# Optimization experiments

Measured on AMD Instinct MI355X. Metric: run time of the kernel, lower is better.

The kernel has to match this reference:

```python
import jax, jax.numpy as jnp
import numpy as np

WINDOW = 7
TOKEN_SELF_ATTN_VALUE = -5e4  # from lucidrains local-attention
LN_EPS = 1e-5


def _layer_norm(x, g, b):
    mu = jnp.mean(x, axis=-1, keepdims=True)
    var = jnp.mean(jnp.square(x - mu), axis=-1, keepdims=True)
    return (x - mu) * jax.lax.rsqrt(var + LN_EPS) * g + b


def _local_attention(q, k, v, window):
    # q,k,v: (b, n, d); shared_qk=True, causal=True, look_backward=1, look_forward=0
    b, n, d = q.shape
    nw = n // window
    scale = d ** -0.5
    # shared_qk: l2-normalize keys (torch F.normalize eps=1e-12)
    k = k / jnp.maximum(jnp.linalg.norm(k, axis=-1, keepdims=True), 1e-12)
    bq = q.reshape(b, nw, window, d) * scale
    bk = k.reshape(b, nw, window, d)
    bv = v.reshape(b, nw, window, d)
    # look_around: previous window + current window -> (b, nw, 2w, d)
    prev_k = jnp.pad(bk, ((0, 0), (1, 0), (0, 0), (0, 0)))[:, :nw]
    prev_v = jnp.pad(bv, ((0, 0), (1, 0), (0, 0), (0, 0)))[:, :nw]
    bk2 = jnp.concatenate([prev_k, bk], axis=2)
    bv2 = jnp.concatenate([prev_v, bv], axis=2)
    # absolute positions; padded positions marked -1
    t = jnp.arange(n).reshape(nw, window)             # (nw, w)
    prev_t = jnp.pad(t, ((1, 0), (0, 0)), constant_values=-1)[:nw]
    tk = jnp.concatenate([prev_t, t], axis=1)          # (nw, 2w)
    sim = jnp.einsum('bnie,bnje->bnij', bq, bk2)       # (b, nw, w, 2w)
    self_mask = t[:, :, None] == tk[:, None, :]
    sim = jnp.where(self_mask, TOKEN_SELF_ATTN_VALUE, sim)
    invalid = (t[:, :, None] < tk[:, None, :]) | (tk[:, None, :] == -1)
    sim = jnp.where(invalid, -jnp.finfo(sim.dtype).max, sim)
    attn = jax.nn.softmax(sim, axis=-1)
    out = jnp.einsum('bnij,bnjd->bnid', attn, bv2)
    return out.reshape(b, n, d)


def setup_inputs() -> dict:
    key = jax.random.key(0)
    ks = jax.random.split(key, 10)
    B, H, W, C = 8, 112, 112, 256
    s = 1.0 / np.sqrt(C)
    return {
        'x': jax.random.normal(ks[0], (B, H, W, C), dtype=jnp.float32),
        'ln_g': jnp.ones((C,), jnp.float32),
        'ln_b': jnp.zeros((C,), jnp.float32),
        'wq_w': jax.random.uniform(ks[1], (C, C), jnp.float32, -s, s),
        'wq_b': jax.random.uniform(ks[2], (C,), jnp.float32, -s, s),
        'wk_w': jax.random.uniform(ks[3], (C, C), jnp.float32, -s, s),
        'wk_b': jax.random.uniform(ks[4], (C,), jnp.float32, -s, s),
        'wv_w': jax.random.uniform(ks[5], (C, C), jnp.float32, -s, s),
        'wv_b': jax.random.uniform(ks[6], (C,), jnp.float32, -s, s),
        'mlp_w': jax.random.uniform(ks[7], (C, C), jnp.float32, -s, s),
        'mlp_b': jax.random.uniform(ks[8], (C,), jnp.float32, -s, s),
    }


def reference(x, ln_g, ln_b, wq_w, wq_b, wk_w, wk_b, wv_w, wv_b, mlp_w, mlp_b):
    B, H, W, C = x.shape
    shift = WINDOW // 2  # int(7/2) = 3
    xs = jnp.roll(x, (shift, shift), axis=(1, 2))
    xs = _layer_norm(xs, ln_g, ln_b)
    flat = xs.reshape(B, H * W, C)
    q = flat @ wq_w.T + wq_b
    k = flat @ wk_w.T + wk_b
    v = flat @ wv_w.T + wv_b
    attn_out = _local_attention(q, k, v, WINDOW).reshape(B, H, W, C)
    x_unshifted = jnp.roll(attn_out, (-shift, -shift), axis=(1, 2))
    residual = x_unshifted + x
    xn = _layer_norm(residual, ln_g, ln_b)  # same LN params (module reused)
    flat2 = xn.reshape(B, H * W, C)
    mlp = jax.nn.gelu(flat2 @ mlp_w.T + mlp_b, approximate=False).reshape(B, H, W, C)
    return mlp + residual
```

## Files before the change

kernel.cpp:

```cpp
#include <hip/hip_runtime.h>

#define NTOK 100352
#define NPB  12544
#define CH   256

typedef unsigned short u16;
typedef float f32x4 __attribute__((ext_vector_type(4)));
typedef short bfrag __attribute__((ext_vector_type(8)));

static __device__ __forceinline__ u16 f2bf(float f) {
    union { float f; unsigned u; } v; v.f = f;
    unsigned r = v.u + 0x7FFFu + ((v.u >> 16) & 1u);
    return (u16)(r >> 16);
}
static __device__ __forceinline__ float bf2f(u16 h) {
    union { unsigned u; float f; } v; v.u = ((unsigned)h) << 16;
    return v.f;
}
static __device__ __forceinline__ unsigned pk2(float a, float b) {
    return (unsigned)f2bf(a) | ((unsigned)f2bf(b) << 16);
}

__global__ __launch_bounds__(256)
void swa_prep(const float* __restrict__ wq, const float* __restrict__ wk,
              const float* __restrict__ wv, const float* __restrict__ wm,
              u16* __restrict__ wcat, u16* __restrict__ wmb)
{
    int i0 = blockIdx.x * 256 + threadIdx.x;
    int stride = gridDim.x * 256;
    for (int i = i0; i < 768 * 256; i += stride) {
        int r = i >> 8, c = i & 255;
        float v;
        if (r < 256)      v = wq[r * 256 + c] * 0.0625f;
        else if (r < 512) v = wk[(r - 256) * 256 + c];
        else              v = wv[(r - 512) * 256 + c];
        wcat[i] = f2bf(v);
    }
    for (int i = i0; i < 256 * 256; i += stride) wmb[i] = f2bf(wm[i]);
}

__global__ __launch_bounds__(256)
void swa_ln(const float* __restrict__ x,
            const float* __restrict__ ln_g, const float* __restrict__ ln_b,
            u16* __restrict__ xn)
{
    const int lane = threadIdx.x & 63;
    const int wid  = threadIdx.x >> 6;
    f32x4 lg = *reinterpret_cast<const f32x4*>(ln_g + lane * 4);
    f32x4 lb = *reinterpret_cast<const f32x4*>(ln_b + lane * 4);

    const int wtok0 = (blockIdx.x * 4 + wid) * 16;
    for (int i = 0; i < 16; ++i) {
        int tok = wtok0 + i;
        int b_  = tok / NPB;
        int rem = tok - b_ * NPB;
        int h = rem / 112, w = rem - h * 112;
        int h0 = h - 3 + ((h < 3) ? 112 : 0);
        int w0 = w - 3 + ((w < 3) ? 112 : 0);
        f32x4 v = *reinterpret_cast<const f32x4*>(x + (size_t)(b_ * NPB + h0 * 112 + w0) * CH + lane * 4);
        float s  = v[0] + v[1] + v[2] + v[3];
        float sq = v[0]*v[0] + v[1]*v[1] + v[2]*v[2] + v[3]*v[3];
        #pragma unroll
        for (int m = 1; m < 64; m <<= 1) { s += __shfl_xor(s, m); sq += __shfl_xor(sq, m); }
        float mu  = s * (1.0f / 256.0f);
        float var = sq * (1.0f / 256.0f) - mu * mu;
        float inv = 1.0f / sqrtf(var + 1e-5f);
        uint2 p;
        p.x = pk2((v[0] - mu) * inv * lg[0] + lb[0], (v[1] - mu) * inv * lg[1] + lb[1]);
        p.y = pk2((v[2] - mu) * inv * lg[2] + lb[2], (v[3] - mu) * inv * lg[3] + lb[3]);
        *reinterpret_cast<uint2*>(xn + (size_t)tok * CH + lane * 4) = p;
    }
}

__global__ __launch_bounds__(256)
void swa_qkv6(const u16* __restrict__ xn, const u16* __restrict__ wcat,
              const float* __restrict__ bq, const float* __restrict__ bk,
              const float* __restrict__ bv,
              u16* __restrict__ qbuf, u16* __restrict__ kbuf, u16* __restrict__ vbuf)
{
    __shared__ u16 wt[2][64 * 64];

    const int tid  = threadIdx.x;
    const int lane = tid & 63;
    const int wid  = tid >> 6;
    const int r16  = lane & 15, g4 = lane >> 4;
    const int swz  = (blockIdx.x & 7) * 98 + (blockIdx.x >> 3);
    const int tok0 = swz * 128;
    const int trow0 = wid * 32;

    bfrag bx[2][8];
    #pragma unroll
    for (int fj = 0; fj < 2; ++fj) {
        const u16* xp = xn + (size_t)(tok0 + trow0 + fj * 16 + r16) * CH + g4 * 8;
        #pragma unroll
        for (int kk = 0; kk < 8; ++kk)
            bx[fj][kk] = *reinterpret_cast<const bfrag*>(xp + kk * 32);
    }

    uint4 wreg[2];
    auto wload = [&](int s) {
        int pp = s >> 2, t = s & 3;
        #pragma unroll
        for (int it = 0; it < 2; ++it) {
            int cid = tid + it * 256;
            int row = cid >> 3, c = cid & 7;
            wreg[it] = *reinterpret_cast<const uint4*>(wcat + (size_t)(pp * 64 + row) * CH + t * 64 + c * 8);
        }
    };
    auto wstore = [&](int p) {
        char* d = (char*)wt[p];
        #pragma unroll
        for (int it = 0; it < 2; ++it) {
            int cid = tid + it * 256;
            int row = cid >> 3, c = cid & 7;
            *reinterpret_cast<uint4*>(d + row * 128 + ((c ^ (row & 7)) << 4)) = wreg[it];
        }
    };

    wload(0); wstore(0);
    __syncthreads();

    f32x4 acc[4][2];
    #pragma unroll
    for (int fi = 0; fi < 4; ++fi) { acc[fi][0] = (f32x4)0.f; acc[fi][1] = (f32x4)0.f; }

    for (int pp = 0; pp < 12; ++pp) {
        #pragma unroll
        for (int t = 0; t < 4; ++t) {
            const int s = pp * 4 + t;
            const int p = s & 1;
            if (s < 47) wload(s + 1);
            const char* wp = (const char*)wt[p];
            #pragma unroll
            for (int kk = 0; kk < 2; ++kk) {
                bfrag af[4];
                #pragma unroll
                for (int fi = 0; fi < 4; ++fi) {
                    int row = fi * 16 + r16;
                    af[fi] = *reinterpret_cast<const bfrag*>(wp + row * 128 + (((kk * 4 + g4) ^ (row & 7)) << 4));
                }
                #pragma unroll
                for (int fi = 0; fi < 4; ++fi)
                    #pragma unroll
                    for (int fj = 0; fj < 2; ++fj)
                        acc[fi][fj] = __builtin_amdgcn_mfma_f32_16x16x32_bf16(af[fi], bx[fj][t * 2 + kk], acc[fi][fj], 0, 0, 0);
            }
            if (t == 3) {
                const int sec = pp >> 2;
                u16* outp = (sec == 0) ? qbuf : (sec == 1) ? kbuf : vbuf;
                const float* bp = (sec == 0) ? bq : (sec == 1) ? bk : bv;
                const float bscale = (sec == 0) ? 0.0625f : 1.0f;
                #pragma unroll
                for (int fi = 0; fi < 4; ++fi) {
                    int chl = (pp & 3) * 64 + fi * 16 + g4 * 4;
                    f32x4 bb = *reinterpret_cast<const f32x4*>(bp + chl);
                    #pragma unroll
                    for (int fj = 0; fj < 2; ++fj) {
                        int tok = tok0 + trow0 + fj * 16 + r16;
                        uint2 pk;
                        pk.x = pk2(acc[fi][fj][0] + bb[0] * bscale, acc[fi][fj][1] + bb[1] * bscale);
                        pk.y = pk2(acc[fi][fj][2] + bb[2] * bscale, acc[fi][fj][3] + bb[3] * bscale);
                        *reinterpret_cast<uint2*>(outp + (size_t)tok * CH + chl) = pk;
                        acc[fi][fj] = (f32x4)0.f;
                    }
                }
            }
            if (s < 47) wstore(p ^ 1);
            __syncthreads();
        }
    }
}

__global__ __launch_bounds__(256)
void swa_attn(const u16* qbuf, const u16* kbuf, const u16* vbuf, u16* obuf)
{
    __shared__ float plds[4][16][17];
    const int tid  = threadIdx.x;
    const int lane = tid & 63;
    const int wid  = tid >> 6;
    const int win  = blockIdx.x * 4 + wid;
    const int iw   = win % 1792;
    const int base = win * 7;
    const int r16  = lane & 15;
    const int g4   = lane >> 4;

    int qrow = base + r16; if (qrow > NTOK - 1) qrow = NTOK - 1;
    int krow = base - 7 + r16; if (krow < 0) krow = 0;
    const u16* qp = qbuf + (size_t)qrow * CH + g4 * 8;
    const u16* kp = kbuf + (size_t)krow * CH + g4 * 8;

    bfrag kf[8];
    #pragma unroll
    for (int kk = 0; kk < 8; ++kk) kf[kk] = *reinterpret_cast<const bfrag*>(kp + kk * 32);
    float sq = 0.f;
    #pragma unroll
    for (int kk = 0; kk < 8; ++kk)
        #pragma unroll
        for (int e = 0; e < 8; ++e) { float kv = bf2f((u16)kf[kk][e]); sq += kv * kv; }
    sq += __shfl_xor(sq, 16); sq += __shfl_xor(sq, 32);
    float invk = 1.0f / fmaxf(sqrtf(sq), 1e-12f);

    f32x4 s4 = {0.f, 0.f, 0.f, 0.f};
    #pragma unroll
    for (int kk = 0; kk < 8; ++kk) {
        bfrag a = *reinterpret_cast<const bfrag*>(qp + kk * 32);
        s4 = __builtin_amdgcn_mfma_f32_16x16x32_bf16(a, kf[kk], s4, 0, 0, 0);
    }

    const int  j     = r16;
    const bool first = (iw == 0);
    #pragma unroll
    for (int rr = 0; rr < 4; ++rr) {
        int i = g4 * 4 + rr;
        float s = s4[rr] * invk;
        if (j == i + 7) s = -5.0e4f;
        if (j > i + 7 || j >= 14 || (first && j < 7)) s = -3.0e38f;
        s4[rr] = s;
    }
    f32x4 mx = s4;
    #pragma unroll
    for (int off = 8; off; off >>= 1) {
        #pragma unroll
        for (int rr = 0; rr < 4; ++rr) mx[rr] = fmaxf(mx[rr], __shfl_xor(mx[rr], off));
    }
    f32x4 p;
    #pragma unroll
    for (int rr = 0; rr < 4; ++rr) p[rr] = __expf(s4[rr] - mx[rr]);
    f32x4 sm = p;
    #pragma unroll
    for (int off = 8; off; off >>= 1) {
        #pragma unroll
        for (int rr = 0; rr < 4; ++rr) sm[rr] += __shfl_xor(sm[rr], off);
    }
    #pragma unroll
    for (int rr = 0; rr < 4; ++rr) plds[wid][g4 * 4 + rr][j] = p[rr] / sm[rr];
    __syncthreads();

    f32x4 zero4 = {0.f, 0.f, 0.f, 0.f};
    f32x4 oa[7];
    #pragma unroll
    for (int i = 0; i < 7; ++i) oa[i] = zero4;
    for (int jj = 0; jj < 14; ++jj) {
        int vrow = base - 7 + jj;
        if (vrow < 0) vrow = 0;
        ushort4 vr = *reinterpret_cast<const ushort4*>(vbuf + (size_t)vrow * CH + lane * 4);
        f32x4 vvv; vvv[0] = bf2f(vr.x); vvv[1] = bf2f(vr.y); vvv[2] = bf2f(vr.z); vvv[3] = bf2f(vr.w);
        #pragma unroll
        for (int i = 0; i < 7; ++i) {
            float pp = plds[wid][i][jj];
            oa[i][0] += pp * vvv[0]; oa[i][1] += pp * vvv[1];
            oa[i][2] += pp * vvv[2]; oa[i][3] += pp * vvv[3];
        }
    }
    #pragma unroll
    for (int i = 0; i < 7; ++i) {
        ushort4 o; o.x = f2bf(oa[i][0]); o.y = f2bf(oa[i][1]); o.z = f2bf(oa[i][2]); o.w = f2bf(oa[i][3]);
        *reinterpret_cast<ushort4*>(obuf + (size_t)(base + i) * CH + lane * 4) = o;
    }
}

__global__ __launch_bounds__(256)
void swa_mlp4(const float* __restrict__ x, const u16* __restrict__ abuf,
              const float* __restrict__ ln_g, const float* __restrict__ ln_b,
              const u16* __restrict__ wmb, const float* __restrict__ mbias,
              float* __restrict__ out)
{
    __shared__ u16   xs[32][264];
    __shared__ float rsd[32][260];
    __shared__ float bias[256];
    const int tid  = threadIdx.x;
    const int lane = tid & 63;
    const int wid  = tid >> 6;
    const int tok0 = blockIdx.x * 32;
    const int r16  = lane & 15;
    const int g4   = lane >> 4;

    if (tid < 256) bias[tid] = mbias[tid];
    f32x4 lg = *reinterpret_cast<const f32x4*>(ln_g + lane * 4);
    f32x4 lb = *reinterpret_cast<const f32x4*>(ln_b + lane * 4);

    for (int it = 0; it < 8; ++it) {
        int tt  = wid * 8 + it;
        int tok = tok0 + tt;
        int b_  = tok / NPB, rem = tok - b_ * NPB;
        int h = rem / 112, w = rem - h * 112;
        int hs = h + 3;  if (hs >= 112) hs -= 112;
        int ws_ = w + 3; if (ws_ >= 112) ws_ -= 112;
        const u16* arow = abuf + (size_t)(b_ * NPB + hs * 112 + ws_) * CH;
        ushort4 av = *reinterpret_cast<const ushort4*>(arow + lane * 4);
        f32x4 xv = *reinterpret_cast<const f32x4*>(x + (size_t)tok * CH + lane * 4);
        f32x4 rv;
        rv[0] = xv[0] + bf2f(av.x); rv[1] = xv[1] + bf2f(av.y);
        rv[2] = xv[2] + bf2f(av.z); rv[3] = xv[3] + bf2f(av.w);
        *reinterpret_cast<f32x4*>(&rsd[tt][lane * 4]) = rv;
        float s  = rv[0] + rv[1] + rv[2] + rv[3];
        float sq = rv[0]*rv[0] + rv[1]*rv[1] + rv[2]*rv[2] + rv[3]*rv[3];
        #pragma unroll
        for (int m = 32; m; m >>= 1) { s += __shfl_xor(s, m); sq += __shfl_xor(sq, m); }
        float mu  = s * (1.0f / 256.0f);
        float var = sq * (1.0f / 256.0f) - mu * mu;
        float inv = 1.0f / sqrtf(var + 1e-5f);
        ushort4 o;
        o.x = f2bf((rv[0] - mu) * inv * lg[0] + lb[0]);
        o.y = f2bf((rv[1] - mu) * inv * lg[1] + lb[1]);
        o.z = f2bf((rv[2] - mu) * inv * lg[2] + lb[2]);
        o.w = f2bf((rv[3] - mu) * inv * lg[3] + lb[3]);
        *reinterpret_cast<ushort4*>(&xs[tt][lane * 4]) = o;
    }
    __syncthreads();

    f32x4 acc[4][2];
    #pragma unroll
    for (int i = 0; i < 4; ++i) { acc[i][0] = (f32x4)0.f; acc[i][1] = (f32x4)0.f; }

    #pragma unroll
    for (int kk = 0; kk < 8; ++kk) {
        bfrag b0 = *reinterpret_cast<const bfrag*>(&xs[r16][kk * 32 + g4 * 8]);
        bfrag b1 = *reinterpret_cast<const bfrag*>(&xs[16 + r16][kk * 32 + g4 * 8]);
        #pragma unroll
        for (int ct = 0; ct < 4; ++ct) {
            bfrag wf = *reinterpret_cast<const bfrag*>(wmb + (size_t)(wid * 64 + ct * 16 + r16) * CH + kk * 32 + g4 * 8);
            acc[ct][0] = __builtin_amdgcn_mfma_f32_16x16x32_bf16(wf, b0, acc[ct][0], 0, 0, 0);
            acc[ct][1] = __builtin_amdgcn_mfma_f32_16x16x32_bf16(wf, b1, acc[ct][1], 0, 0, 0);
        }
    }

    #pragma unroll
    for (int ct = 0; ct < 4; ++ct) {
        int ch = wid * 64 + ct * 16 + g4 * 4;
        f32x4 bb = *reinterpret_cast<const f32x4*>(&bias[ch]);
        #pragma unroll
        for (int rt = 0; rt < 2; ++rt) {
            int tokL = rt * 16 + r16;
            f32x4 rb = *reinterpret_cast<const f32x4*>(&rsd[tokL][ch]);
            f32x4 vv;
            #pragma unroll
            for (int rr = 0; rr < 4; ++rr) {
                float val = acc[ct][rt][rr] + bb[rr];
                vv[rr] = 0.5f * val * (1.0f + erff(val * 0.70710678118654752f)) + rb[rr];
            }
            *reinterpret_cast<f32x4*>(out + (size_t)(tok0 + tokL) * CH + ch) = vv;
        }
    }
}

extern "C" void kernel_launch(void* const* d_in, const int* in_sizes, int n_in,
                              void* d_out, int out_size, void* d_ws, size_t ws_size,
                              hipStream_t stream)
{
    const float* x     = (const float*)d_in[0];
    const float* ln_g  = (const float*)d_in[1];
    const float* ln_b  = (const float*)d_in[2];
    const float* wq_w  = (const float*)d_in[3];
    const float* wq_b  = (const float*)d_in[4];
    const float* wk_w  = (const float*)d_in[5];
    const float* wk_b  = (const float*)d_in[6];
    const float* wv_w  = (const float*)d_in[7];
    const float* wv_b  = (const float*)d_in[8];
    const float* mlp_w = (const float*)d_in[9];
    const float* mlp_b = (const float*)d_in[10];

    char* ws = (char*)d_ws;
    u16* wcat = (u16*)ws;
    u16* wmb  = (u16*)(ws + 393216);
    u16* xnq  = (u16*)(ws + 524288);
    u16* kbuf = (u16*)d_out;
    u16* vbuf = (u16*)d_out + (size_t)NTOK * CH;

    swa_prep <<<256,  256, 0, stream>>>(wq_w, wk_w, wv_w, mlp_w, wcat, wmb);
    swa_ln   <<<1568, 256, 0, stream>>>(x, ln_g, ln_b, xnq);
    swa_qkv6 <<<784,  256, 0, stream>>>(xnq, wcat, wq_b, wk_b, wv_b, xnq, kbuf, vbuf);
    swa_attn <<<3584, 256, 0, stream>>>(xnq, kbuf, vbuf, xnq);
    swa_mlp4 <<<3136, 256, 0, stream>>>(x, xnq, ln_g, ln_b, wmb, mlp_b, (float*)d_out);
}
```

Baseline: 305.2 us.

## Restructure QKV GEMM with direct global-to-LDS weight staging and 512-thread blocks

```diff
diff --git a/kernel.cpp b/kernel.cpp
--- a/kernel.cpp
+++ b/kernel.cpp
@@ -19,6 +19,11 @@
 }
 static __device__ __forceinline__ unsigned pk2(float a, float b) {
     return (unsigned)f2bf(a) | ((unsigned)f2bf(b) << 16);
+}
+static __device__ __forceinline__ void gl16(const u16* g, u16* l) {
+    __builtin_amdgcn_global_load_lds(
+        (const __attribute__((address_space(1))) void*)g,
+        (__attribute__((address_space(3))) void*)l, 16, 0, 0);
 }
 
 __global__ __launch_bounds__(256)
@@ -72,102 +77,106 @@
     }
 }
 
-__global__ __launch_bounds__(256)
-void swa_qkv6(const u16* __restrict__ xn, const u16* __restrict__ wcat,
+#define QSTEP(KH, SPP, DOSTAGE)                                                        \
+    {                                                                                  \
+        if (DOSTAGE) {                                                                 \
+            const int spp_ = (SPP);                                                    \
+            _Pragma("unroll")                                                          \
+            for (int it = 0; it < 2; ++it) {                                           \
+                int o   = (tid + it * 512) * 16;                                       \
+                int row = o >> 8;                                                      \
+                int cp  = (o >> 4) & 15;                                               \
+                int c   = (cp & 8) | ((cp & 7) ^ (row & 7));                           \
+                const u16* gp = wcat + (size_t)(spp_ * 64 + row) * CH + ((KH) ^ 1) * 128 + c * 8; \
+                gl16(gp, (u16*)wt[(KH) ^ 1] + o / 2);                                  \
+            }                                                                          \
+        }                                                                              \
+        const char* wp = (const char*)wt[(KH)];                                        \
+        _Pragma("unroll")                                                              \
+        for (int kk = 0; kk < 4; ++kk) {                                               \
+            bfrag af[2];                                                               \
+            _Pragma("unroll")                                                          \
+            for (int fi = 0; fi < 2; ++fi) {                                           \
+                int row = wch * 32 + fi * 16 + r16;                                    \
+                int cc  = kk * 4 + g4;                                                 \
+                int cp  = (cc & 8) | ((cc & 7) ^ (r16 & 7));                           \
+                af[fi]  = *reinterpret_cast<const bfrag*>(wp + row * 256 + cp * 16);   \
+            }                                                                          \
+            _Pragma("unroll")                                                          \
+            for (int fi = 0; fi < 2; ++fi)                                             \
+                _Pragma("unroll")                                                      \
+                for (int fj = 0; fj < 2; ++fj)                                         \
+                    acc[fi][fj] = __builtin_amdgcn_mfma_f32_16x16x32_bf16(af[fi], bx[fj][(KH) * 4 + kk], acc[fi][fj], 0, 0, 0); \
+        }                                                                              \
+    }
+
+__global__ __launch_bounds__(512)
+void swa_qkv7(const u16* __restrict__ xn, const u16* __restrict__ wcat,
               const float* __restrict__ bq, const float* __restrict__ bk,
               const float* __restrict__ bv,
               u16* __restrict__ qbuf, u16* __restrict__ kbuf, u16* __restrict__ vbuf)
 {
-    __shared__ u16 wt[2][64 * 64];
+    __shared__ u16 wt[2][64 * 128];
 
     const int tid  = threadIdx.x;
     const int lane = tid & 63;
     const int wid  = tid >> 6;
     const int r16  = lane & 15, g4 = lane >> 4;
+    const int wch  = wid & 1;
+    const int wtk  = wid >> 1;
     const int swz  = (blockIdx.x & 7) * 98 + (blockIdx.x >> 3);
     const int tok0 = swz * 128;
-    const int trow0 = wid * 32;
+    const int trow0 = wtk * 32;
 
     bfrag bx[2][8];
     #pragma unroll
     for (int fj = 0; fj < 2; ++fj) {
         const u16* xp = xn + (size_t)(tok0 + trow0 + fj * 16 + r16) * CH + g4 * 8;
         #pragma unroll
-        for (int kk = 0; kk < 8; ++kk)
-            bx[fj][kk] = *reinterpret_cast<const bfrag*>(xp + kk * 32);
-    }
-
-    uint4 wreg[2];
-    auto wload = [&](int s) {
-        int pp = s >> 2, t = s & 3;
-        #pragma unroll
-        for (int it = 0; it < 2; ++it) {
-            int cid = tid + it * 256;
-            int row = cid >> 3, c = cid & 7;
-            wreg[it] = *reinterpret_cast<const uint4*>(wcat + (size_t)(pp * 64 + row) * CH + t * 64 + c * 8);
-        }
-    };
-    auto wstore = [&](int p) {
-        char* d = (char*)wt[p];
-        #pragma unroll
-        for (int it = 0; it < 2; ++it) {
-            int cid = tid + it * 256;
-            int row = cid >> 3, c = cid & 7;
-            *reinterpret_cast<uint4*>(d + row * 128 + ((c ^ (row & 7)) << 4)) = wreg[it];
-        }
-    };
-
-    wload(0); wstore(0);
+        for (int kb = 0; kb < 8; ++kb)
+            bx[fj][kb] = *reinterpret_cast<const bfrag*>(xp + kb * 32);
+    }
+
+    #pragma unroll
+    for (int it = 0; it < 2; ++it) {
+        int o   = (tid + it * 512) * 16;
+        int row = o >> 8;
+        int cp  = (o >> 4) & 15;
+        int c   = (cp & 8) | ((cp & 7) ^ (row & 7));
+        gl16(wcat + (size_t)row * CH + c * 8, (u16*)wt[0] + o / 2);
+    }
     __syncthreads();
 
-    f32x4 acc[4][2];
-    #pragma unroll
-    for (int fi = 0; fi < 4; ++fi) { acc[fi][0] = (f32x4)0.f; acc[fi][1] = (f32x4)0.f; }
+    f32x4 acc[2][2];
+    #pragma unroll
+    for (int fi = 0; fi < 2; ++fi) { acc[fi][0] = (f32x4)0.f; acc[fi][1] = (f32x4)0.f; }
 
     for (int pp = 0; pp < 12; ++pp) {
-        #pragma unroll
-        for (int t = 0; t < 4; ++t) {
-            const int s = pp * 4 + t;
-            const int p = s & 1;
-            if (s < 47) wload(s + 1);
-            const char* wp = (const char*)wt[p];
+        QSTEP(0, pp, true);
+        __syncthreads();
+        QSTEP(1, pp + 1, pp < 11);
+
+        {
+            const int sec = pp >> 2;
+            u16* outp = (sec == 0) ? qbuf : (sec == 1) ? kbuf : vbuf;
+            const float* bp = (sec == 0) ? bq : (sec == 1) ? bk : bv;
+            const float bsc = (sec == 0) ? 0.0625f : 1.0f;
             #pragma unroll
-            for (int kk = 0; kk < 2; ++kk) {
-                bfrag af[4];
+            for (int fi = 0; fi < 2; ++fi) {
+                int chl = (pp & 3) * 64 + wch * 32 + fi * 16 + g4 * 4;
+                f32x4 bb = *reinterpret_cast<const f32x4*>(bp + chl);
                 #pragma unroll
-                for (int fi = 0; fi < 4; ++fi) {
-                    int row = fi * 16 + r16;
-                    af[fi] = *reinterpret_cast<const bfrag*>(wp + row * 128 + (((kk * 4 + g4) ^ (row & 7)) << 4));
-                }
-                #pragma unroll
-                for (int fi = 0; fi < 4; ++fi)
-                    #pragma unroll
-                    for (int fj = 0; fj < 2; ++fj)
-                        acc[fi][fj] = __builtin_amdgcn_mfma_f32_16x16x32_bf16(af[fi], bx[fj][t * 2 + kk], acc[fi][fj], 0, 0, 0);
-            }
-            if (t == 3) {
-                const int sec = pp >> 2;
-                u16* outp = (sec == 0) ? qbuf : (sec == 1) ? kbuf : vbuf;
-                const float* bp = (sec == 0) ? bq : (sec == 1) ? bk : bv;
-                const float bscale = (sec == 0) ? 0.0625f : 1.0f;
-                #pragma unroll
-                for (int fi = 0; fi < 4; ++fi) {
-                    int chl = (pp & 3) * 64 + fi * 16 + g4 * 4;
-                    f32x4 bb = *reinterpret_cast<const f32x4*>(bp + chl);
-                    #pragma unroll
-                    for (int fj = 0; fj < 2; ++fj) {
-                        int tok = tok0 + trow0 + fj * 16 + r16;
-                        uint2 pk;
-                        pk.x = pk2(acc[fi][fj][0] + bb[0] * bscale, acc[fi][fj][1] + bb[1] * bscale);
-                        pk.y = pk2(acc[fi][fj][2] + bb[2] * bscale, acc[fi][fj][3] + bb[3] * bscale);
-                        *reinterpret_cast<uint2*>(outp + (size_t)tok * CH + chl) = pk;
-                        acc[fi][fj] = (f32x4)0.f;
-                    }
+                for (int fj = 0; fj < 2; ++fj) {
+                    int tok = tok0 + trow0 + fj * 16 + r16;
+                    uint2 pk;
+                    pk.x = pk2(acc[fi][fj][0] + bb[0] * bsc, acc[fi][fj][1] + bb[1] * bsc);
+                    pk.y = pk2(acc[fi][fj][2] + bb[2] * bsc, acc[fi][fj][3] + bb[3] * bsc);
+                    *reinterpret_cast<uint2*>(outp + (size_t)tok * CH + chl) = pk;
+                    acc[fi][fj] = (f32x4)0.f;
                 }
             }
-            if (s < 47) wstore(p ^ 1);
-            __syncthreads();
         }
+        __syncthreads();
     }
 }
 
@@ -369,7 +378,7 @@
 
     swa_prep <<<256,  256, 0, stream>>>(wq_w, wk_w, wv_w, mlp_w, wcat, wmb);
     swa_ln   <<<1568, 256, 0, stream>>>(x, ln_g, ln_b, xnq);
-    swa_qkv6 <<<784,  256, 0, stream>>>(xnq, wcat, wq_b, wk_b, wv_b, xnq, kbuf, vbuf);
+    swa_qkv7 <<<784,  512, 0, stream>>>(xnq, wcat, wq_b, wk_b, wv_b, xnq, kbuf, vbuf);
     swa_attn <<<3584, 256, 0, stream>>>(xnq, kbuf, vbuf, xnq);
     swa_mlp4 <<<3136, 256, 0, stream>>>(x, xnq, ln_g, ln_b, wmb, mlp_b, (float*)d_out);
 }
```

Result: faster. 282.4 us (-7.5%).

## Fuse LayerNorm into QKV projection and hold full weight section in LDS

Applied to the files above, without the earlier changes.

```diff
diff --git a/kernel.cpp b/kernel.cpp
--- a/kernel.cpp
+++ b/kernel.cpp
@@ -19,6 +19,11 @@
 }
 static __device__ __forceinline__ unsigned pk2(float a, float b) {
     return (unsigned)f2bf(a) | ((unsigned)f2bf(b) << 16);
+}
+static __device__ __forceinline__ void gl16(const u16* g, u16* l) {
+    __builtin_amdgcn_global_load_lds(
+        (const __attribute__((address_space(1))) void*)g,
+        (__attribute__((address_space(3))) void*)l, 16, 0, 0);
 }
 
 __global__ __launch_bounds__(256)
@@ -39,134 +44,116 @@
     for (int i = i0; i < 256 * 256; i += stride) wmb[i] = f2bf(wm[i]);
 }
 
-__global__ __launch_bounds__(256)
-void swa_ln(const float* __restrict__ x,
-            const float* __restrict__ ln_g, const float* __restrict__ ln_b,
-            u16* __restrict__ xn)
-{
-    const int lane = threadIdx.x & 63;
-    const int wid  = threadIdx.x >> 6;
-    f32x4 lg = *reinterpret_cast<const f32x4*>(ln_g + lane * 4);
-    f32x4 lb = *reinterpret_cast<const f32x4*>(ln_b + lane * 4);
-
-    const int wtok0 = (blockIdx.x * 4 + wid) * 16;
-    for (int i = 0; i < 16; ++i) {
-        int tok = wtok0 + i;
-        int b_  = tok / NPB;
-        int rem = tok - b_ * NPB;
-        int h = rem / 112, w = rem - h * 112;
-        int h0 = h - 3 + ((h < 3) ? 112 : 0);
-        int w0 = w - 3 + ((w < 3) ? 112 : 0);
-        f32x4 v = *reinterpret_cast<const f32x4*>(x + (size_t)(b_ * NPB + h0 * 112 + w0) * CH + lane * 4);
-        float s  = v[0] + v[1] + v[2] + v[3];
-        float sq = v[0]*v[0] + v[1]*v[1] + v[2]*v[2] + v[3]*v[3];
-        #pragma unroll
-        for (int m = 1; m < 64; m <<= 1) { s += __shfl_xor(s, m); sq += __shfl_xor(sq, m); }
-        float mu  = s * (1.0f / 256.0f);
-        float var = sq * (1.0f / 256.0f) - mu * mu;
-        float inv = 1.0f / sqrtf(var + 1e-5f);
-        uint2 p;
-        p.x = pk2((v[0] - mu) * inv * lg[0] + lb[0], (v[1] - mu) * inv * lg[1] + lb[1]);
-        p.y = pk2((v[2] - mu) * inv * lg[2] + lb[2], (v[3] - mu) * inv * lg[3] + lb[3]);
-        *reinterpret_cast<uint2*>(xn + (size_t)tok * CH + lane * 4) = p;
-    }
-}
-
-__global__ __launch_bounds__(256)
-void swa_qkv6(const u16* __restrict__ xn, const u16* __restrict__ wcat,
+__global__ __launch_bounds__(512)
+void swa_qkv8(const float* __restrict__ x,
+              const float* __restrict__ ln_g, const float* __restrict__ ln_b,
+              const u16* __restrict__ wcat,
               const float* __restrict__ bq, const float* __restrict__ bk,
               const float* __restrict__ bv,
               u16* __restrict__ qbuf, u16* __restrict__ kbuf, u16* __restrict__ vbuf)
 {
-    __shared__ u16 wt[2][64 * 64];
+    __shared__ u16 wt[256 * 256];
 
     const int tid  = threadIdx.x;
     const int lane = tid & 63;
     const int wid  = tid >> 6;
     const int r16  = lane & 15, g4 = lane >> 4;
-    const int swz  = (blockIdx.x & 7) * 98 + (blockIdx.x >> 3);
-    const int tok0 = swz * 128;
-    const int trow0 = wid * 32;
+    const int sec   = blockIdx.x / 392;
+    const int strip = blockIdx.x % 392;
+    const int tok0  = strip * 256 + wid * 32;
+
+    #pragma unroll
+    for (int rr = 0; rr < 16; ++rr) {
+        int o   = (tid + rr * 512) * 16;
+        int row = o >> 9;
+        int cp  = (o >> 4) & 31;
+        int c   = (cp & 24) | ((cp & 7) ^ (row & 7));
+        gl16(wcat + (size_t)(sec * 256 + row) * CH + c * 8, wt + o / 2);
+    }
 
     bfrag bx[2][8];
     #pragma unroll
     for (int fj = 0; fj < 2; ++fj) {
-        const u16* xp = xn + (size_t)(tok0 + trow0 + fj * 16 + r16) * CH + g4 * 8;
-        #pragma unroll
-        for (int kk = 0; kk < 8; ++kk)
-            bx[fj][kk] = *reinterpret_cast<const bfrag*>(xp + kk * 32);
-    }
-
-    uint4 wreg[2];
-    auto wload = [&](int s) {
-        int pp = s >> 2, t = s & 3;
-        #pragma unroll
-        for (int it = 0; it < 2; ++it) {
-            int cid = tid + it * 256;
-            int row = cid >> 3, c = cid & 7;
-            wreg[it] = *reinterpret_cast<const uint4*>(wcat + (size_t)(pp * 64 + row) * CH + t * 64 + c * 8);
-        }
-    };
-    auto wstore = [&](int p) {
-        char* d = (char*)wt[p];
-        #pragma unroll
-        for (int it = 0; it < 2; ++it) {
-            int cid = tid + it * 256;
-            int row = cid >> 3, c = cid & 7;
-            *reinterpret_cast<uint4*>(d + row * 128 + ((c ^ (row & 7)) << 4)) = wreg[it];
-        }
-    };
-
-    wload(0); wstore(0);
+        int tok = tok0 + fj * 16 + r16;
+        int b_  = tok / NPB, rem = tok - b_ * NPB;
+        int h = rem / 112, w = rem - h * 112;
+        int h0 = h - 3 + ((h < 3) ? 112 : 0);
+        int w0 = w - 3 + ((w < 3) ? 112 : 0);
+        const float* rp = x + (size_t)(b_ * NPB + h0 * 112 + w0) * CH + g4 * 8;
+        f32x4 xv[16];
+        #pragma unroll
+        for (int kb = 0; kb < 8; ++kb) {
+            xv[kb * 2]     = *reinterpret_cast<const f32x4*>(rp + kb * 32);
+            xv[kb * 2 + 1] = *reinterpret_cast<const f32x4*>(rp + kb * 32 + 4);
+        }
+        float s = 0.f, sq = 0.f;
+        #pragma unroll
+        for (int q = 0; q < 16; ++q) {
+            s  += xv[q][0] + xv[q][1] + xv[q][2] + xv[q][3];
+            sq += xv[q][0]*xv[q][0] + xv[q][1]*xv[q][1] + xv[q][2]*xv[q][2] + xv[q][3]*xv[q][3];
+        }
+        s  += __shfl_xor(s, 16); sq += __shfl_xor(sq, 16);
+        s  += __shfl_xor(s, 32); sq += __shfl_xor(sq, 32);
+        float mu  = s * (1.0f / 256.0f);
+        float var = sq * (1.0f / 256.0f) - mu * mu;
+        float inv = 1.0f / sqrtf(var + 1e-5f);
+        #pragma unroll
+        for (int kb = 0; kb < 8; ++kb) {
+            const float* gp = ln_g + kb * 32 + g4 * 8;
+            const float* bp = ln_b + kb * 32 + g4 * 8;
+            f32x4 g0 = *reinterpret_cast<const f32x4*>(gp);
+            f32x4 g1 = *reinterpret_cast<const f32x4*>(gp + 4);
+            f32x4 b0 = *reinterpret_cast<const f32x4*>(bp);
+            f32x4 b1 = *reinterpret_cast<const f32x4*>(bp + 4);
+            f32x4 a0 = xv[kb * 2], a1 = xv[kb * 2 + 1];
+            union { unsigned u[4]; bfrag f; } cv;
+            cv.u[0] = pk2((a0[0]-mu)*inv*g0[0]+b0[0], (a0[1]-mu)*inv*g0[1]+b0[1]);
+            cv.u[1] = pk2((a0[2]-mu)*inv*g0[2]+b0[2], (a0[3]-mu)*inv*g0[3]+b0[3]);
+            cv.u[2] = pk2((a1[0]-mu)*inv*g1[0]+b1[0], (a1[1]-mu)*inv*g1[1]+b1[1]);
+            cv.u[3] = pk2((a1[2]-mu)*inv*g1[2]+b1[2], (a1[3]-mu)*inv*g1[3]+b1[3]);
+            bx[fj][kb] = cv.f;
+        }
+    }
+
+    u16*         outp = (sec == 0) ? qbuf : (sec == 1) ? kbuf : vbuf;
+    const float* bsp  = (sec == 0) ? bq : (sec == 1) ? bk : bv;
+    const float  bsc  = (sec == 0) ? 0.0625f : 1.0f;
+
     __syncthreads();
 
-    f32x4 acc[4][2];
-    #pragma unroll
-    for (int fi = 0; fi < 4; ++fi) { acc[fi][0] = (f32x4)0.f; acc[fi][1] = (f32x4)0.f; }
-
-    for (int pp = 0; pp < 12; ++pp) {
-        #pragma unroll
-        for (int t = 0; t < 4; ++t) {
-            const int s = pp * 4 + t;
-            const int p = s & 1;
-            if (s < 47) wload(s + 1);
-            const char* wp = (const char*)wt[p];
+    #pragma unroll
+    for (int ctg = 0; ctg < 4; ++ctg) {
+        f32x4 acc[4][2];
+        #pragma unroll
+        for (int ct = 0; ct < 4; ++ct) { acc[ct][0] = (f32x4)0.f; acc[ct][1] = (f32x4)0.f; }
+        #pragma unroll
+        for (int kk = 0; kk < 8; ++kk) {
+            bfrag af[4];
             #pragma unroll
-            for (int kk = 0; kk < 2; ++kk) {
-                bfrag af[4];
-                #pragma unroll
-                for (int fi = 0; fi < 4; ++fi) {
-                    int row = fi * 16 + r16;
-                    af[fi] = *reinterpret_cast<const bfrag*>(wp + row * 128 + (((kk * 4 + g4) ^ (row & 7)) << 4));
-                }
-                #pragma unroll
-                for (int fi = 0; fi < 4; ++fi)
-                    #pragma unroll
-                    for (int fj = 0; fj < 2; ++fj)
-                        acc[fi][fj] = __builtin_amdgcn_mfma_f32_16x16x32_bf16(af[fi], bx[fj][t * 2 + kk], acc[fi][fj], 0, 0, 0);
+            for (int ct = 0; ct < 4; ++ct) {
+                int row = ctg * 64 + ct * 16 + r16;
+                int cc  = kk * 4 + g4;
+                int cp  = (cc & 24) | ((cc & 7) ^ (row & 7));
+                af[ct]  = *reinterpret_cast<const bfrag*>((const char*)wt + row * 512 + cp * 16);
             }
-            if (t == 3) {
-                const int sec = pp >> 2;
-                u16* outp = (sec == 0) ? qbuf : (sec == 1) ? kbuf : vbuf;
-                const float* bp = (sec == 0) ? bq : (sec == 1) ? bk : bv;
-                const float bscale = (sec == 0) ? 0.0625f : 1.0f;
-                #pragma unroll
-                for (int fi = 0; fi < 4; ++fi) {
-                    int chl = (pp & 3) * 64 + fi * 16 + g4 * 4;
-                    f32x4 bb = *reinterpret_cast<const f32x4*>(bp + chl);
-                    #pragma unroll
-                    for (int fj = 0; fj < 2; ++fj) {
-                        int tok = tok0 + trow0 + fj * 16 + r16;
-                        uint2 pk;
-                        pk.x = pk2(acc[fi][fj][0] + bb[0] * bscale, acc[fi][fj][1] + bb[1] * bscale);
-                        pk.y = pk2(acc[fi][fj][2] + bb[2] * bscale, acc[fi][fj][3] + bb[3] * bscale);
-                        *reinterpret_cast<uint2*>(outp + (size_t)tok * CH + chl) = pk;
-                        acc[fi][fj] = (f32x4)0.f;
-                    }
-                }
+            #pragma unroll
+            for (int ct = 0; ct < 4; ++ct) {
+                acc[ct][0] = __builtin_amdgcn_mfma_f32_16x16x32_bf16(af[ct], bx[0][kk], acc[ct][0], 0, 0, 0);
+                acc[ct][1] = __builtin_amdgcn_mfma_f32_16x16x32_bf16(af[ct], bx[1][kk], acc[ct][1], 0, 0, 0);
             }
-            if (s < 47) wstore(p ^ 1);
-            __syncthreads();
+        }
+        #pragma unroll
+        for (int ct = 0; ct < 4; ++ct) {
+            int ch = ctg * 64 + ct * 16 + g4 * 4;
+            f32x4 bb = *reinterpret_cast<const f32x4*>(bsp + ch);
+            #pragma unroll
+            for (int fj = 0; fj < 2; ++fj) {
+                int tok = tok0 + fj * 16 + r16;
+                uint2 pkk;
+                pkk.x = pk2(acc[ct][fj][0] + bb[0] * bsc, acc[ct][fj][1] + bb[1] * bsc);
+                pkk.y = pk2(acc[ct][fj][2] + bb[2] * bsc, acc[ct][fj][3] + bb[3] * bsc);
+                *reinterpret_cast<uint2*>(outp + (size_t)tok * CH + ch) = pkk;
+            }
         }
     }
 }
@@ -363,13 +350,12 @@
     char* ws = (char*)d_ws;
     u16* wcat = (u16*)ws;
     u16* wmb  = (u16*)(ws + 393216);
-    u16* xnq  = (u16*)(ws + 524288);
+    u16* qbuf = (u16*)(ws + 524288);
     u16* kbuf = (u16*)d_out;
     u16* vbuf = (u16*)d_out + (size_t)NTOK * CH;
 
     swa_prep <<<256,  256, 0, stream>>>(wq_w, wk_w, wv_w, mlp_w, wcat, wmb);
-    swa_ln   <<<1568, 256, 0, stream>>>(x, ln_g, ln_b, xnq);
-    swa_qkv6 <<<784,  256, 0, stream>>>(xnq, wcat, wq_b, wk_b, wv_b, xnq, kbuf, vbuf);
-    swa_attn <<<3584, 256, 0, stream>>>(xnq, kbuf, vbuf, xnq);
-    swa_mlp4 <<<3136, 256, 0, stream>>>(x, xnq, ln_g, ln_b, wmb, mlp_b, (float*)d_out);
-}
+    swa_qkv8 <<<1176, 512, 0, stream>>>(x, ln_g, ln_b, wcat, wq_b, wk_b, wv_b, qbuf, kbuf, vbuf);
+    swa_attn <<<3584, 256, 0, stream>>>(qbuf, kbuf, vbuf, qbuf);
+    swa_mlp4 <<<3136, 256, 0, stream>>>(x, qbuf, ln_g, ln_b, wmb, mlp_b, (float*)d_out);
+}
```

After: 259.2 us. -15.1%, faster.

## Split QKV projection into K/V and in-place Q kernels with LDS-resident weights

Applied to the files above, without the earlier changes.

```diff
diff --git a/kernel.cpp b/kernel.cpp
--- a/kernel.cpp
+++ b/kernel.cpp
@@ -19,6 +19,11 @@
 }
 static __device__ __forceinline__ unsigned pk2(float a, float b) {
     return (unsigned)f2bf(a) | ((unsigned)f2bf(b) << 16);
+}
+static __device__ __forceinline__ void gl16(const u16* g, u16* l) {
+    __builtin_amdgcn_global_load_lds(
+        (const __attribute__((address_space(1))) void*)g,
+        (__attribute__((address_space(3))) void*)l, 16, 0, 0);
 }
 
 __global__ __launch_bounds__(256)
@@ -72,101 +77,150 @@
     }
 }
 
-__global__ __launch_bounds__(256)
-void swa_qkv6(const u16* __restrict__ xn, const u16* __restrict__ wcat,
-              const float* __restrict__ bq, const float* __restrict__ bk,
-              const float* __restrict__ bv,
-              u16* __restrict__ qbuf, u16* __restrict__ kbuf, u16* __restrict__ vbuf)
-{
-    __shared__ u16 wt[2][64 * 64];
+__global__ __launch_bounds__(512)
+void swa_kv(const u16* __restrict__ xn, const u16* __restrict__ wcat,
+            const float* __restrict__ bk, const float* __restrict__ bv,
+            u16* __restrict__ kbuf, u16* __restrict__ vbuf)
+{
+    __shared__ u16 wt[128 * 256];
 
     const int tid  = threadIdx.x;
     const int lane = tid & 63;
     const int wid  = tid >> 6;
     const int r16  = lane & 15, g4 = lane >> 4;
-    const int swz  = (blockIdx.x & 7) * 98 + (blockIdx.x >> 3);
-    const int tok0 = swz * 128;
-    const int trow0 = wid * 32;
+    const int swz   = (blockIdx.x & 7) * 196 + (blockIdx.x >> 3);
+    const int type  = swz / 392;
+    const int strip = swz % 392;
+    const int sec   = 1 + (type >> 1);
+    const int half  = type & 1;
+    const int tok0w = strip * 256 + wid * 32;
+    const int wrow0 = sec * 256 + half * 128;
+
+    #pragma unroll
+    for (int rr2 = 0; rr2 < 8; ++rr2) {
+        int o   = (tid + rr2 * 512) * 16;
+        int row = o >> 9;
+        int cp  = (o >> 4) & 31;
+        int c   = (cp & 24) | ((cp & 7) ^ (row & 7));
+        gl16(wcat + (size_t)(wrow0 + row) * CH + c * 8, wt + o / 2);
+    }
 
     bfrag bx[2][8];
     #pragma unroll
     for (int fj = 0; fj < 2; ++fj) {
-        const u16* xp = xn + (size_t)(tok0 + trow0 + fj * 16 + r16) * CH + g4 * 8;
-        #pragma unroll
-        for (int kk = 0; kk < 8; ++kk)
-            bx[fj][kk] = *reinterpret_cast<const bfrag*>(xp + kk * 32);
-    }
-
-    uint4 wreg[2];
-    auto wload = [&](int s) {
-        int pp = s >> 2, t = s & 3;
-        #pragma unroll
-        for (int it = 0; it < 2; ++it) {
-            int cid = tid + it * 256;
-            int row = cid >> 3, c = cid & 7;
-            wreg[it] = *reinterpret_cast<const uint4*>(wcat + (size_t)(pp * 64 + row) * CH + t * 64 + c * 8);
-        }
-    };
-    auto wstore = [&](int p) {
-        char* d = (char*)wt[p];
-        #pragma unroll
-        for (int it = 0; it < 2; ++it) {
-            int cid = tid + it * 256;
-            int row = cid >> 3, c = cid & 7;
-            *reinterpret_cast<uint4*>(d + row * 128 + ((c ^ (row & 7)) << 4)) = wreg[it];
-        }
-    };
-
-    wload(0); wstore(0);
+        const u16* xp = xn + (size_t)(tok0w + fj * 16 + r16) * CH + g4 * 8;
+        #pragma unroll
+        for (int kb = 0; kb < 8; ++kb)
+            bx[fj][kb] = *reinterpret_cast<const bfrag*>(xp + kb * 32);
+    }
+
+    u16*         outp = (sec == 1) ? kbuf : vbuf;
+    const float* bsp  = (sec == 1) ? bk : bv;
+
     __syncthreads();
 
-    f32x4 acc[4][2];
-    #pragma unroll
-    for (int fi = 0; fi < 4; ++fi) { acc[fi][0] = (f32x4)0.f; acc[fi][1] = (f32x4)0.f; }
-
-    for (int pp = 0; pp < 12; ++pp) {
-        #pragma unroll
-        for (int t = 0; t < 4; ++t) {
-            const int s = pp * 4 + t;
-            const int p = s & 1;
-            if (s < 47) wload(s + 1);
-            const char* wp = (const char*)wt[p];
-            #pragma unroll
-            for (int kk = 0; kk < 2; ++kk) {
-                bfrag af[4];
-                #pragma unroll
-                for (int fi = 0; fi < 4; ++fi) {
-                    int row = fi * 16 + r16;
-                    af[fi] = *reinterpret_cast<const bfrag*>(wp + row * 128 + (((kk * 4 + g4) ^ (row & 7)) << 4));
-                }
-                #pragma unroll
-                for (int fi = 0; fi < 4; ++fi)
-                    #pragma unroll
-                    for (int fj = 0; fj < 2; ++fj)
-                        acc[fi][fj] = __builtin_amdgcn_mfma_f32_16x16x32_bf16(af[fi], bx[fj][t * 2 + kk], acc[fi][fj], 0, 0, 0);
-            }
-            if (t == 3) {
-                const int sec = pp >> 2;
-                u16* outp = (sec == 0) ? qbuf : (sec == 1) ? kbuf : vbuf;
-                const float* bp = (sec == 0) ? bq : (sec == 1) ? bk : bv;
-                const float bscale = (sec == 0) ? 0.0625f : 1.0f;
-                #pragma unroll
-                for (int fi = 0; fi < 4; ++fi) {
-                    int chl = (pp & 3) * 64 + fi * 16 + g4 * 4;
-                    f32x4 bb = *reinterpret_cast<const f32x4*>(bp + chl);
-                    #pragma unroll
-                    for (int fj = 0; fj < 2; ++fj) {
-                        int tok = tok0 + trow0 + fj * 16 + r16;
-                        uint2 pk;
-                        pk.x = pk2(acc[fi][fj][0] + bb[0] * bscale, acc[fi][fj][1] + bb[1] * bscale);
-                        pk.y = pk2(acc[fi][fj][2] + bb[2] * bscale, acc[fi][fj][3] + bb[3] * bscale);
-                        *reinterpret_cast<uint2*>(outp + (size_t)tok * CH + chl) = pk;
-                        acc[fi][fj] = (f32x4)0.f;
-                    }
-                }
-            }
-            if (s < 47) wstore(p ^ 1);
-            __syncthreads();
+    #pragma unroll
+    for (int p = 0; p < 4; ++p) {
+        f32x4 acc[2][2];
+        #pragma unroll
+        for (int ct = 0; ct < 2; ++ct) { acc[ct][0] = (f32x4)0.f; acc[ct][1] = (f32x4)0.f; }
+        #pragma unroll
+        for (int kk = 0; kk < 8; ++kk) {
+            bfrag af[2];
+            #pragma unroll
+            for (int ct = 0; ct < 2; ++ct) {
+                int row = p * 32 + ct * 16 + r16;
+                int cc  = kk * 4 + g4;
+                int cp  = (cc & 24) | ((cc & 7) ^ (row & 7));
+                af[ct]  = *reinterpret_cast<const bfrag*>((const char*)wt + row * 512 + cp * 16);
+            }
+            #pragma unroll
+            for (int ct = 0; ct < 2; ++ct) {
+                acc[ct][0] = __builtin_amdgcn_mfma_f32_16x16x32_bf16(af[ct], bx[0][kk], acc[ct][0], 0, 0, 0);
+                acc[ct][1] = __builtin_amdgcn_mfma_f32_16x16x32_bf16(af[ct], bx[1][kk], acc[ct][1], 0, 0, 0);
+            }
+        }
+        #pragma unroll
+        for (int ct = 0; ct < 2; ++ct) {
+            int ch = half * 128 + p * 32 + ct * 16 + g4 * 4;
+            f32x4 bb = *reinterpret_cast<const f32x4*>(bsp + ch);
+            #pragma unroll
+            for (int fj = 0; fj < 2; ++fj) {
+                int tok = tok0w + fj * 16 + r16;
+                uint2 pkk;
+                pkk.x = pk2(acc[ct][fj][0] + bb[0], acc[ct][fj][1] + bb[1]);
+                pkk.y = pk2(acc[ct][fj][2] + bb[2], acc[ct][fj][3] + bb[3]);
+                *reinterpret_cast<uint2*>(outp + (size_t)tok * CH + ch) = pkk;
+            }
+        }
+    }
+}
+
+__global__ __launch_bounds__(512)
+void swa_q(u16* xnq, const u16* __restrict__ wcat, const float* __restrict__ bq)
+{
+    __shared__ u16 wt[256 * 256];
+
+    const int tid  = threadIdx.x;
+    const int lane = tid & 63;
+    const int wid  = tid >> 6;
+    const int r16  = lane & 15, g4 = lane >> 4;
+    const int strip = (blockIdx.x & 7) * 49 + (blockIdx.x >> 3);
+    const int tok0w = strip * 256 + wid * 32;
+
+    #pragma unroll
+    for (int rr2 = 0; rr2 < 16; ++rr2) {
+        int o   = (tid + rr2 * 512) * 16;
+        int row = o >> 9;
+        int cp  = (o >> 4) & 31;
+        int c   = (cp & 24) | ((cp & 7) ^ (row & 7));
+        gl16(wcat + (size_t)row * CH + c * 8, wt + o / 2);
+    }
+
+    bfrag bx[2][8];
+    #pragma unroll
+    for (int fj = 0; fj < 2; ++fj) {
+        const u16* xp = xnq + (size_t)(tok0w + fj * 16 + r16) * CH + g4 * 8;
+        #pragma unroll
+        for (int kb = 0; kb < 8; ++kb)
+            bx[fj][kb] = *reinterpret_cast<const bfrag*>(xp + kb * 32);
+    }
+
+    __syncthreads();
+
+    #pragma unroll
+    for (int p = 0; p < 8; ++p) {
+        f32x4 acc[2][2];
+        #pragma unroll
+        for (int ct = 0; ct < 2; ++ct) { acc[ct][0] = (f32x4)0.f; acc[ct][1] = (f32x4)0.f; }
+        #pragma unroll
+        for (int kk = 0; kk < 8; ++kk) {
+            bfrag af[2];
+            #pragma unroll
+            for (int ct = 0; ct < 2; ++ct) {
+                int row = p * 32 + ct * 16 + r16;
+                int cc  = kk * 4 + g4;
+                int cp  = (cc & 24) | ((cc & 7) ^ (row & 7));
+                af[ct]  = *reinterpret_cast<const bfrag*>((const char*)wt + row * 512 + cp * 16);
+            }
+            #pragma unroll
+            for (int ct = 0; ct < 2; ++ct) {
+                acc[ct][0] = __builtin_amdgcn_mfma_f32_16x16x32_bf16(af[ct], bx[0][kk], acc[ct][0], 0, 0, 0);
+                acc[ct][1] = __builtin_amdgcn_mfma_f32_16x16x32_bf16(af[ct], bx[1][kk], acc[ct][1], 0, 0, 0);
+            }
+        }
+        #pragma unroll
+        for (int ct = 0; ct < 2; ++ct) {
+            int ch = p * 32 + ct * 16 + g4 * 4;
+            f32x4 bb = *reinterpret_cast<const f32x4*>(bq + ch);
+            #pragma unroll
+            for (int fj = 0; fj < 2; ++fj) {
+                int tok = tok0w + fj * 16 + r16;
+                uint2 pkk;
+                pkk.x = pk2(acc[ct][fj][0] + bb[0] * 0.0625f, acc[ct][fj][1] + bb[1] * 0.0625f);
+                pkk.y = pk2(acc[ct][fj][2] + bb[2] * 0.0625f, acc[ct][fj][3] + bb[3] * 0.0625f);
+                *reinterpret_cast<uint2*>(xnq + (size_t)tok * CH + ch) = pkk;
+            }
         }
     }
 }
@@ -369,7 +423,8 @@
 
     swa_prep <<<256,  256, 0, stream>>>(wq_w, wk_w, wv_w, mlp_w, wcat, wmb);
     swa_ln   <<<1568, 256, 0, stream>>>(x, ln_g, ln_b, xnq);
-    swa_qkv6 <<<784,  256, 0, stream>>>(xnq, wcat, wq_b, wk_b, wv_b, xnq, kbuf, vbuf);
+    swa_kv   <<<1568, 512, 0, stream>>>(xnq, wcat, wk_b, wv_b, kbuf, vbuf);
+    swa_q    <<<392,  512, 0, stream>>>(xnq, wcat, wq_b);
     swa_attn <<<3584, 256, 0, stream>>>(xnq, kbuf, vbuf, xnq);
     swa_mlp4 <<<3136, 256, 0, stream>>>(x, xnq, ln_g, ln_b, wmb, mlp_b, (float*)d_out);
 }
```

New measurement: 269.6 us. 11.7% less time.
